# Performance work log

Hardware: AMD Instinct MI355X
Metric: run time of the kernel (lower is better)

The kernel has to match this reference:

```python
import jax, jax.numpy as jnp
import numpy as np

COMMITMENT_COST = 0.25
NUM_EMBEDDINGS = 1024
EMBEDDING_DIM = 512  # win_size(8) * num_pellets(64)


def setup_inputs() -> dict:
    key = jax.random.key(0)
    k1, k2 = jax.random.split(key)
    inputs = jax.random.normal(k1, (64, 256, EMBEDDING_DIM), dtype=jnp.float32)
    # matches torch init: uniform_(-1/K, 1/K)
    lim = 1.0 / NUM_EMBEDDINGS
    emb_weight = jax.random.uniform(k2, (NUM_EMBEDDINGS, EMBEDDING_DIM),
                                    dtype=jnp.float32, minval=-lim, maxval=lim)
    return {"inputs": inputs, "emb_weight": emb_weight}


def reference(inputs, emb_weight):
    batch_size = inputs.shape[0]
    input_shape = inputs.shape
    flat = inputs.reshape(-1, EMBEDDING_DIM)  # [N, D]

    distances = (jnp.sum(flat * flat, axis=1, keepdims=True)
                 + jnp.sum(emb_weight * emb_weight, axis=1)
                 - 2.0 * flat @ emb_weight.T)
    encoding_indices = jnp.argmin(distances, axis=1)  # [N]

    # gather instead of one-hot matmul (same math)
    quantized = emb_weight[encoding_indices].reshape(input_shape)

    e_latent_loss = jnp.mean((jax.lax.stop_gradient(quantized) - inputs) ** 2)
    q_latent_loss = jnp.mean((quantized - jax.lax.stop_gradient(inputs)) ** 2)
    loss_vq = q_latent_loss + COMMITMENT_COST * e_latent_loss

    # straight-through estimator
    quantized = inputs + jax.lax.stop_gradient(quantized - inputs)

    encoding_indices = encoding_indices.reshape(batch_size, -1)
    return loss_vq, quantized, encoding_indices
```

## Files before the change

kernel.cpp:

```cpp
#include <hip/hip_runtime.h>
#include <cfloat>

#define NROWS  16384
#define DIM    512
#define KC     1024
#define QELEMS (NROWS * DIM)

#define NSPLIT 8
#define CHUNKS 132

typedef float  floatx4 __attribute__((ext_vector_type(4)));
typedef _Float16 half8 __attribute__((ext_vector_type(8)));
typedef _Float16 half4 __attribute__((ext_vector_type(4)));

__global__ __launch_bounds__(256) void prep_kernel(const float* __restrict__ A,
                                                   const float* __restrict__ E,
                                                   float* __restrict__ xsq,
                                                   float* __restrict__ esq,
                                                   _Float16* __restrict__ ah,
                                                   _Float16* __restrict__ al,
                                                   _Float16* __restrict__ eh,
                                                   _Float16* __restrict__ el,
                                                   unsigned long long* __restrict__ packed,
                                                   float* __restrict__ out) {
    if (blockIdx.x == 0 && threadIdx.x == 0) out[0] = 0.f;
    const int wave = threadIdx.x >> 6, lane = threadIdx.x & 63;
    const bool isA = blockIdx.x < (NROWS / 4);
    const int row = (isA ? blockIdx.x : blockIdx.x - NROWS / 4) * 4 + wave;
    const float* M = isA ? A : E;
    const float scale = isA ? 2048.0f : 65536.0f;

    const float4* Mr = (const float4*)(M + (size_t)row * DIM);
    float4 va = Mr[lane];
    float4 vb = Mr[lane + 64];
    float s = 0.f;
    s += va.x*va.x + va.y*va.y + va.z*va.z + va.w*va.w;
    s += vb.x*vb.x + vb.y*vb.y + vb.z*vb.z + vb.w*vb.w;
    #pragma unroll
    for (int off = 32; off; off >>= 1) s += __shfl_down(s, off, 64);
    if (lane == 0) {
        if (isA) { xsq[row] = s; packed[row] = ~0ULL; }
        else     { esq[row] = s; }
    }

    float xa[4] = {va.x, va.y, va.z, va.w}, xb[4] = {vb.x, vb.y, vb.z, vb.w};
    half4 ha, la, hb, lb;
    #pragma unroll
    for (int e = 0; e < 4; ++e) {
        float t = xa[e] * scale;
        _Float16 h = (_Float16)t;
        ha[e] = h; la[e] = (_Float16)(t - (float)h);
        t = xb[e] * scale;
        h = (_Float16)t;
        hb[e] = h; lb[e] = (_Float16)(t - (float)h);
    }
    _Float16* hr = (isA ? ah : eh) + (size_t)row * DIM;
    _Float16* lr = (isA ? al : el) + (size_t)row * DIM;
    ((half4*)hr)[lane]      = ha;
    ((half4*)lr)[lane]      = la;
    ((half4*)hr)[lane + 64] = hb;
    ((half4*)lr)[lane + 64] = lb;
}

__global__ __launch_bounds__(256) void mfma_argmin_kernel(const _Float16* __restrict__ ah,
                                                          const _Float16* __restrict__ al,
                                                          const _Float16* __restrict__ eh,
                                                          const _Float16* __restrict__ el,
                                                          const float* __restrict__ esq,
                                                          const float* __restrict__ xsq,
                                                          unsigned long long* __restrict__ packed) {
    __shared__ half8 AhT[2][4 * CHUNKS], AlT[2][4 * CHUNKS];
    __shared__ half8 EhT[2][4 * CHUNKS], ElT[2][4 * CHUNKS];
    __shared__ float redv[128][2];
    __shared__ int   redi[128][2];

    const int tid = threadIdx.x;
    const int lane = tid & 63, wave = tid >> 6;
    const int wm = wave >> 1, wn = wave & 1;
    const int tx = lane & 15, qd = lane >> 4;
    const int bm = blockIdx.x & 127, bn = blockIdx.x >> 7;
    const int m0 = bm * 128, c0 = bn * 128;

    const int srow = tid >> 2, skq = tid & 3;
    const _Float16* gA  = ah + (size_t)(m0 + srow) * DIM + skq * 8;
    const _Float16* gAl = al + (size_t)(m0 + srow) * DIM + skq * 8;
    const _Float16* gE  = eh + (size_t)(c0 + srow) * DIM + skq * 8;
    const _Float16* gEl = el + (size_t)(c0 + srow) * DIM + skq * 8;
    const int cw0 = skq * CHUNKS + srow, cw1 = cw0 + 64;

    floatx4 acc[4][4];
    #pragma unroll
    for (int i = 0; i < 4; ++i)
        #pragma unroll
        for (int j = 0; j < 4; ++j) acc[i][j] = (floatx4){0.f, 0.f, 0.f, 0.f};

    half8 rA0  = *(const half8*)(gA);
    half8 rA1  = *(const half8*)(gA  + 64 * DIM);
    half8 rL0  = *(const half8*)(gAl);
    half8 rL1  = *(const half8*)(gAl + 64 * DIM);
    half8 rE0  = *(const half8*)(gE);
    half8 rE1  = *(const half8*)(gE  + 64 * DIM);
    half8 rF0  = *(const half8*)(gEl);
    half8 rF1  = *(const half8*)(gEl + 64 * DIM);
    AhT[0][cw0] = rA0; AhT[0][cw1] = rA1;
    AlT[0][cw0] = rL0; AlT[0][cw1] = rL1;
    EhT[0][cw0] = rE0; EhT[0][cw1] = rE1;
    ElT[0][cw0] = rF0; ElT[0][cw1] = rF1;

    #pragma unroll 1
    for (int kt = 0; kt < DIM / 32; ++kt) {
        const int cur = kt & 1, nxt = cur ^ 1;
        const int kb = (kt + 1) * 32;
        if (kt < DIM / 32 - 1) {
            rA0 = *(const half8*)(gA  + kb);
            rA1 = *(const half8*)(gA  + 64 * DIM + kb);
            rL0 = *(const half8*)(gAl + kb);
            rL1 = *(const half8*)(gAl + 64 * DIM + kb);
            rE0 = *(const half8*)(gE  + kb);
            rE1 = *(const half8*)(gE  + 64 * DIM + kb);
            rF0 = *(const half8*)(gEl + kb);
            rF1 = *(const half8*)(gEl + 64 * DIM + kb);
        }
        __syncthreads();

        half8 fa[4], fbh[4], fbl[4];
        #pragma unroll
        for (int i = 0; i < 4; ++i)
            fa[i] = AhT[cur][qd * CHUNKS + wm * 64 + i * 16 + tx];
        #pragma unroll
        for (int j = 0; j < 4; ++j) {
            fbh[j] = EhT[cur][qd * CHUNKS + wn * 64 + j * 16 + tx];
            fbl[j] = ElT[cur][qd * CHUNKS + wn * 64 + j * 16 + tx];
        }
        #pragma unroll
        for (int i = 0; i < 4; ++i)
            #pragma unroll
            for (int j = 0; j < 4; ++j)
                acc[i][j] = __builtin_amdgcn_mfma_f32_16x16x32_f16(fa[i], fbh[j], acc[i][j], 0, 0, 0);
        #pragma unroll
        for (int i = 0; i < 4; ++i)
            #pragma unroll
            for (int j = 0; j < 4; ++j)
                acc[i][j] = __builtin_amdgcn_mfma_f32_16x16x32_f16(fa[i], fbl[j], acc[i][j], 0, 0, 0);
        #pragma unroll
        for (int i = 0; i < 4; ++i)
            fa[i] = AlT[cur][qd * CHUNKS + wm * 64 + i * 16 + tx];
        #pragma unroll
        for (int i = 0; i < 4; ++i)
            #pragma unroll
            for (int j = 0; j < 4; ++j)
                acc[i][j] = __builtin_amdgcn_mfma_f32_16x16x32_f16(fa[i], fbh[j], acc[i][j], 0, 0, 0);

        if (kt < DIM / 32 - 1) {
            AhT[nxt][cw0] = rA0; AhT[nxt][cw1] = rA1;
            AlT[nxt][cw0] = rL0; AlT[nxt][cw1] = rL1;
            EhT[nxt][cw0] = rE0; EhT[nxt][cw1] = rE1;
            ElT[nxt][cw0] = rF0; ElT[nxt][cw1] = rF1;
        }
    }

    float sqe_v[4];
    #pragma unroll
    for (int j = 0; j < 4; ++j) sqe_v[j] = esq[c0 + wn * 64 + j * 16 + tx];
    #pragma unroll
    for (int i = 0; i < 4; ++i) {
        #pragma unroll
        for (int r = 0; r < 4; ++r) {
            int rl = wm * 64 + i * 16 + qd * 4 + r;
            float sx = xsq[m0 + rl];
            float bvv = FLT_MAX; int bii = 0x7fffffff;
            #pragma unroll
            for (int j = 0; j < 4; ++j) {
                float S = sx + sqe_v[j];
                float s = S - acc[i][j][r] * (1.0f / 67108864.0f);
                int c = c0 + wn * 64 + j * 16 + tx;
                if (s < bvv || (s == bvv && c < bii)) { bvv = s; bii = c; }
            }
            #pragma unroll
            for (int md = 1; md < 16; md <<= 1) {
                float ov = __shfl_xor(bvv, md, 64);
                int   oc = __shfl_xor(bii, md, 64);
                if (ov < bvv || (ov == bvv && oc < bii)) { bvv = ov; bii = oc; }
            }
            if (tx == 0) { redv[rl][wn] = bvv; redi[rl][wn] = bii; }
        }
    }
    __syncthreads();
    if (tid < 128) {
        float v0 = redv[tid][0], v1 = redv[tid][1];
        int   i0 = redi[tid][0], i1 = redi[tid][1];
        float v = (v1 < v0) ? v1 : v0;
        int   ix = (v1 < v0) ? i1 : i0;
        unsigned long long pk = ((unsigned long long)__float_as_uint(v) << 32)
                              | (unsigned int)ix;
        atomicMin(&packed[m0 + tid], pk);
    }
}

__global__ __launch_bounds__(256) void finalize_kernel(const float* __restrict__ E,
                                                       const unsigned long long* __restrict__ packed,
                                                       float* __restrict__ out) {
    float* q = out + 1;
    float* idxF = out + 1 + QELEMS;
    const int tid = threadIdx.x;
    const int r0 = blockIdx.x * 64;

    __shared__ int sidx[64];
    if (tid < 64) {
        unsigned long long pk = packed[r0 + tid];
        int idx = (int)(unsigned int)(pk & 0xFFFFFFFFull);
        float sc = __uint_as_float((unsigned int)(pk >> 32));
        sidx[tid] = idx;
        idxF[r0 + tid] = (float)idx;
        #pragma unroll
        for (int off = 32; off; off >>= 1) sc += __shfl_down(sc, off, 64);
        if (tid == 0) atomicAdd(out, sc * (1.25f / (float)QELEMS));
    }
    __syncthreads();

    #pragma unroll 4
    for (int it = 0; it < 32; ++it) {
        int flat = it * 256 + tid;
        int row = flat >> 7;
        int d4  = (flat & 127) * 4;
        int idx = sidx[row];
        float4 e = *(const float4*)(E + (size_t)idx * DIM + d4);
        *(float4*)(q + (size_t)(r0 + row) * DIM + d4) = e;
    }
}

extern "C" void kernel_launch(void* const* d_in, const int* in_sizes, int n_in,
                              void* d_out, int out_size, void* d_ws, size_t ws_size,
                              hipStream_t stream) {
    const float* A = (const float*)d_in[0];
    const float* E = (const float*)d_in[1];
    float* out = (float*)d_out;

    unsigned long long* packed = (unsigned long long*)d_ws;
    float*    esq  = (float*)(packed + NROWS);
    float*    xsq  = esq + KC;
    _Float16* eh   = (_Float16*)(xsq + NROWS);
    _Float16* el   = eh + (size_t)KC * DIM;
    _Float16* ah   = el + (size_t)KC * DIM;
    _Float16* al   = ah + (size_t)NROWS * DIM;

    prep_kernel<<<NROWS / 4 + KC / 4, 256, 0, stream>>>(A, E, xsq, esq, ah, al, eh, el, packed, out);
    mfma_argmin_kernel<<<(NROWS / 128) * NSPLIT, 256, 0, stream>>>(
        ah, al, eh, el, esq, xsq, packed);
    finalize_kernel<<<NROWS / 64, 256, 0, stream>>>(E, packed, out);
}
```

Baseline: 167.3 us.

## Load A-low fragments directly from global and single-buffer shared tiles

Result: no change. 168.2 us (+0.6%).

```diff
diff --git a/kernel.cpp b/kernel.cpp
--- a/kernel.cpp
+++ b/kernel.cpp
@@ -7,7 +7,7 @@
 #define QELEMS (NROWS * DIM)
 
 #define NSPLIT 8
-#define CHUNKS 132
+#define CHUNKS 130
 
 typedef float  floatx4 __attribute__((ext_vector_type(4)));
 typedef _Float16 half8 __attribute__((ext_vector_type(8)));
@@ -69,8 +69,7 @@
                                                           const float* __restrict__ esq,
                                                           const float* __restrict__ xsq,
                                                           unsigned long long* __restrict__ packed) {
-    __shared__ half8 AhT[2][4 * CHUNKS], AlT[2][4 * CHUNKS];
-    __shared__ half8 EhT[2][4 * CHUNKS], ElT[2][4 * CHUNKS];
+    __shared__ half8 AhT[4 * CHUNKS], EhT[4 * CHUNKS], ElT[4 * CHUNKS];
     __shared__ float redv[128][2];
     __shared__ int   redi[128][2];
 
@@ -83,54 +82,46 @@
 
     const int srow = tid >> 2, skq = tid & 3;
     const _Float16* gA  = ah + (size_t)(m0 + srow) * DIM + skq * 8;
-    const _Float16* gAl = al + (size_t)(m0 + srow) * DIM + skq * 8;
     const _Float16* gE  = eh + (size_t)(c0 + srow) * DIM + skq * 8;
     const _Float16* gEl = el + (size_t)(c0 + srow) * DIM + skq * 8;
     const int cw0 = skq * CHUNKS + srow, cw1 = cw0 + 64;
 
+    const _Float16* gAl = al + (size_t)(m0 + wm * 64 + tx) * DIM + qd * 8;
+
     floatx4 acc[4][4];
     #pragma unroll
     for (int i = 0; i < 4; ++i)
         #pragma unroll
         for (int j = 0; j < 4; ++j) acc[i][j] = (floatx4){0.f, 0.f, 0.f, 0.f};
-
-    half8 rA0  = *(const half8*)(gA);
-    half8 rA1  = *(const half8*)(gA  + 64 * DIM);
-    half8 rL0  = *(const half8*)(gAl);
-    half8 rL1  = *(const half8*)(gAl + 64 * DIM);
-    half8 rE0  = *(const half8*)(gE);
-    half8 rE1  = *(const half8*)(gE  + 64 * DIM);
-    half8 rF0  = *(const half8*)(gEl);
-    half8 rF1  = *(const half8*)(gEl + 64 * DIM);
-    AhT[0][cw0] = rA0; AhT[0][cw1] = rA1;
-    AlT[0][cw0] = rL0; AlT[0][cw1] = rL1;
-    EhT[0][cw0] = rE0; EhT[0][cw1] = rE1;
-    ElT[0][cw0] = rF0; ElT[0][cw1] = rF1;
 
     #pragma unroll 1
     for (int kt = 0; kt < DIM / 32; ++kt) {
-        const int cur = kt & 1, nxt = cur ^ 1;
-        const int kb = (kt + 1) * 32;
-        if (kt < DIM / 32 - 1) {
-            rA0 = *(const half8*)(gA  + kb);
-            rA1 = *(const half8*)(gA  + 64 * DIM + kb);
-            rL0 = *(const half8*)(gAl + kb);
-            rL1 = *(const half8*)(gAl + 64 * DIM + kb);
-            rE0 = *(const half8*)(gE  + kb);
-            rE1 = *(const half8*)(gE  + 64 * DIM + kb);
-            rF0 = *(const half8*)(gEl + kb);
-            rF1 = *(const half8*)(gEl + 64 * DIM + kb);
-        }
+        const int kb = kt * 32;
+        half8 sA0 = *(const half8*)(gA  + kb);
+        half8 sA1 = *(const half8*)(gA  + 64 * DIM + kb);
+        half8 sE0 = *(const half8*)(gE  + kb);
+        half8 sE1 = *(const half8*)(gE  + 64 * DIM + kb);
+        half8 sF0 = *(const half8*)(gEl + kb);
+        half8 sF1 = *(const half8*)(gEl + 64 * DIM + kb);
+        half8 fal[4];
+        #pragma unroll
+        for (int i = 0; i < 4; ++i)
+            fal[i] = *(const half8*)(gAl + (size_t)(i * 16) * DIM + kb);
+
         __syncthreads();
+        AhT[cw0] = sA0; AhT[cw1] = sA1;
+        EhT[cw0] = sE0; EhT[cw1] = sE1;
+        ElT[cw0] = sF0; ElT[cw1] = sF1;
+        __syncthreads();
 
         half8 fa[4], fbh[4], fbl[4];
         #pragma unroll
         for (int i = 0; i < 4; ++i)
-            fa[i] = AhT[cur][qd * CHUNKS + wm * 64 + i * 16 + tx];
+            fa[i] = AhT[qd * CHUNKS + wm * 64 + i * 16 + tx];
         #pragma unroll
         for (int j = 0; j < 4; ++j) {
-            fbh[j] = EhT[cur][qd * CHUNKS + wn * 64 + j * 16 + tx];
-            fbl[j] = ElT[cur][qd * CHUNKS + wn * 64 + j * 16 + tx];
+            fbh[j] = EhT[qd * CHUNKS + wn * 64 + j * 16 + tx];
+            fbl[j] = ElT[qd * CHUNKS + wn * 64 + j * 16 + tx];
         }
         #pragma unroll
         for (int i = 0; i < 4; ++i)
@@ -144,19 +135,9 @@
                 acc[i][j] = __builtin_amdgcn_mfma_f32_16x16x32_f16(fa[i], fbl[j], acc[i][j], 0, 0, 0);
         #pragma unroll
         for (int i = 0; i < 4; ++i)
-            fa[i] = AlT[cur][qd * CHUNKS + wm * 64 + i * 16 + tx];
-        #pragma unroll
-        for (int i = 0; i < 4; ++i)
             #pragma unroll
             for (int j = 0; j < 4; ++j)
-                acc[i][j] = __builtin_amdgcn_mfma_f32_16x16x32_f16(fa[i], fbh[j], acc[i][j], 0, 0, 0);
-
-        if (kt < DIM / 32 - 1) {
-            AhT[nxt][cw0] = rA0; AhT[nxt][cw1] = rA1;
-            AlT[nxt][cw0] = rL0; AlT[nxt][cw1] = rL1;
-            EhT[nxt][cw0] = rE0; EhT[nxt][cw1] = rE1;
-            ElT[nxt][cw0] = rF0; ElT[nxt][cw1] = rF1;
-        }
+                acc[i][j] = __builtin_amdgcn_mfma_f32_16x16x32_f16(fal[i], fbh[j], acc[i][j], 0, 0, 0);
     }
 
     float sqe_v[4];
```
